# Kernel optimization log

Hardware: AMD Instinct MI355X
Metric: run time of the kernel (lower is better)

Reference implementation:

```python
import math
import jax, jax.numpy as jnp
import numpy as np

B, T, C, HS = 4, 4096, 2048, 128

def setup_inputs() -> dict:
    key = jax.random.key(0)
    k1, k2, k3, k4 = jax.random.split(key, 4)
    x = jax.random.normal(k1, (B, T, C), dtype=jnp.float32)
    # torch Linear init ~ U(-1/sqrt(in), 1/sqrt(in)); normal*0.02 is fine for a numeric baseline
    Wq = jax.random.normal(k2, (C, HS), dtype=jnp.float32) * 0.02
    Wk = jax.random.normal(k3, (C, HS), dtype=jnp.float32) * 0.02
    Wv = jax.random.normal(k4, (C, HS), dtype=jnp.float32) * 0.02
    return {"x": x, "Wq": Wq, "Wk": Wk, "Wv": Wv}

def reference(x, Wq, Wk, Wv):
    # Single-head causal self-attention (dropout in eval mode = identity).
    q = x @ Wq          # [B,T,HS]
    k = x @ Wk          # [B,T,HS]
    v = x @ Wv          # [B,T,HS]
    scale = 1.0 / math.sqrt(HS)
    att = jnp.einsum('bqd,bkd->bqk', q, k) * scale          # [B,T,T]
    causal = jnp.tril(jnp.ones((T, T), dtype=bool))          # [T,T]
    att = jnp.where(causal[None, :, :], att, -jnp.inf)
    att = jax.nn.softmax(att, axis=-1)
    y = jnp.einsum('bqk,bkd->bqd', att, v)                   # [B,T,HS]
    return y
```

## Files before the change

kernel.cpp:

```cpp
#include <hip/hip_runtime.h>
#include <hip/hip_bf16.h>


#define B_  4
#define T_  4096
#define C_  2048
#define HS_ 128

typedef unsigned short u16;
typedef __attribute__((ext_vector_type(8))) short short8;
typedef __attribute__((ext_vector_type(4))) float floatx4;

static __device__ __forceinline__ u16 f2bf(float x) {
  union { float f; unsigned u; } c; c.f = x;
  unsigned r = 0x7fffu + ((c.u >> 16) & 1u);
  return (u16)((c.u + r) >> 16);
}
static __device__ __forceinline__ u16 cvt_elem(float x) { return f2bf(x); }
static __device__ __forceinline__ u16 cvt_elem(u16 x) { return x; }

template <typename ST>
__global__ __launch_bounds__(256) void transpose_kernel(
    const ST* __restrict__ src, u16* __restrict__ dst, int R, int C) {
  __shared__ u16 tile[32][33];
  size_t moff = (size_t)blockIdx.z * (size_t)R * (size_t)C;
  src += moff; dst += moff;
  int c0 = blockIdx.x * 32, r0 = blockIdx.y * 32;
  int tx = threadIdx.x, ty = threadIdx.y;
#pragma unroll
  for (int i = 0; i < 4; ++i)
    tile[ty + 8 * i][tx] = cvt_elem(src[(size_t)(r0 + ty + 8 * i) * C + (c0 + tx)]);
  __syncthreads();
#pragma unroll
  for (int i = 0; i < 4; ++i)
    dst[(size_t)(c0 + ty + 8 * i) * R + (r0 + tx)] = tile[tx][ty + 8 * i];
}

#define GBM 128
#define GBK 64
#define LPAD 72

__global__ __launch_bounds__(256) void qkv_gemm_kernel(
    const float* __restrict__ X, const u16* __restrict__ WT3,
    u16* __restrict__ qkv) {
  __shared__ u16 Xs[GBM][LPAD];
  __shared__ u16 Ws[HS_][LPAD];
  int z = blockIdx.y;
  const u16* Wt = WT3 + (size_t)z * HS_ * C_;
  u16* outp = qkv + (size_t)z * ((size_t)B_ * T_ * HS_);
  int t = threadIdx.x;
  int wv = t >> 6, lane = t & 63;
  int l15 = lane & 15, hi = lane >> 4;
  int wm = (wv & 1) * 64, wn = (wv >> 1) * 64;
  size_t mbase = (size_t)blockIdx.x * GBM;

  floatx4 acc[4][4];
#pragma unroll
  for (int i = 0; i < 4; ++i)
#pragma unroll
    for (int j = 0; j < 4; ++j) acc[i][j] = (floatx4){0.f, 0.f, 0.f, 0.f};

  for (int kt = 0; kt < C_ / GBK; ++kt) {
#pragma unroll
    for (int i = 0; i < 4; ++i) {
      int id = i * 256 + t;
      int m = id >> 3, c = id & 7;
      const float* sp = &X[(mbase + m) * C_ + kt * GBK + c * 8];
      short8 v;
#pragma unroll
      for (int j = 0; j < 8; ++j) v[j] = (short)f2bf(sp[j]);
      *(short8*)&Xs[m][c * 8] = v;
    }
#pragma unroll
    for (int i = 0; i < 4; ++i) {
      int id = i * 256 + t;
      int n = id >> 3, c = id & 7;
      *(short8*)&Ws[n][c * 8] =
          *(const short8*)&Wt[(size_t)n * C_ + kt * GBK + c * 8];
    }
    __syncthreads();
#pragma unroll
    for (int ks = 0; ks < 2; ++ks) {
      short8 af[4], bf[4];
#pragma unroll
      for (int mt = 0; mt < 4; ++mt)
        af[mt] = *(const short8*)&Xs[wm + mt * 16 + l15][ks * 32 + hi * 8];
#pragma unroll
      for (int nt = 0; nt < 4; ++nt)
        bf[nt] = *(const short8*)&Ws[wn + nt * 16 + l15][ks * 32 + hi * 8];
#pragma unroll
      for (int mt = 0; mt < 4; ++mt)
#pragma unroll
        for (int nt = 0; nt < 4; ++nt)
          acc[mt][nt] = __builtin_amdgcn_mfma_f32_16x16x32_bf16(
              af[mt], bf[nt], acc[mt][nt], 0, 0, 0);
    }
    __syncthreads();
  }
#pragma unroll
  for (int mt = 0; mt < 4; ++mt)
#pragma unroll
    for (int nt = 0; nt < 4; ++nt)
#pragma unroll
      for (int r = 0; r < 4; ++r) {
        size_t row = mbase + wm + mt * 16 + hi * 4 + r;
        int col = wn + nt * 16 + l15;
        outp[row * HS_ + col] = f2bf(acc[mt][nt][r]);
      }
}

#define BQ 64
#define BKV 64
#define CHUNK 16

template <bool WRITE_PARTIAL>
static __device__ __forceinline__ void flash_body(
    const u16* __restrict__ q, const u16* __restrict__ k,
    const u16* __restrict__ vT, float* __restrict__ outO,
    float* __restrict__ Mp, float* __restrict__ Lp,
    int b, int qb, int kb0, int kb1, int slot) {
  __shared__ u16 Ks[BKV][136];
  __shared__ u16 Vs[HS_][72];
  __shared__ u16 Ps[BQ][72];
  int t = threadIdx.x;
  int wv = t >> 6, lane = t & 63, l15 = lane & 15, hi = lane >> 4;

  const float sc = 0.08838834764831845f * 1.4426950408889634f;

  short8 qf[4];
  {
    const u16* qrow = q + (size_t)(b * T_ + qb * BQ + wv * 16 + l15) * HS_;
#pragma unroll
    for (int ks = 0; ks < 4; ++ks)
      qf[ks] = *(const short8*)(qrow + ks * 32 + hi * 8);
  }

  floatx4 of[8];
#pragma unroll
  for (int dt = 0; dt < 8; ++dt) of[dt] = (floatx4){0.f, 0.f, 0.f, 0.f};
  float m_run[4], l_run[4];
#pragma unroll
  for (int r = 0; r < 4; ++r) { m_run[r] = -__builtin_inff(); l_run[r] = 0.f; }

  const u16* kbase = k + (size_t)b * T_ * HS_;
  const u16* vbase = vT + (size_t)b * HS_ * T_;

  for (int kb = kb0; kb <= kb1; ++kb) {
#pragma unroll
    for (int i = 0; i < 4; ++i) {
      int id = i * 256 + t;
      int n = id >> 4, c = id & 15;
      *(short8*)&Ks[n][c * 8] =
          *(const short8*)&kbase[(size_t)(kb * BKV + n) * HS_ + c * 8];
    }
#pragma unroll
    for (int i = 0; i < 4; ++i) {
      int id = i * 256 + t;
      int d = id >> 3, c = id & 7;
      *(short8*)&Vs[d][c * 8] =
          *(const short8*)&vbase[(size_t)d * T_ + kb * BKV + c * 8];
    }
    __syncthreads();

    floatx4 sf[4];
#pragma unroll
    for (int nt = 0; nt < 4; ++nt) {
      floatx4 s = (floatx4){0.f, 0.f, 0.f, 0.f};
#pragma unroll
      for (int ks = 0; ks < 4; ++ks) {
        short8 bfrag = *(const short8*)&Ks[nt * 16 + l15][ks * 32 + hi * 8];
        s = __builtin_amdgcn_mfma_f32_16x16x32_bf16(qf[ks], bfrag, s, 0, 0, 0);
      }
      sf[nt] = s;
    }

    float sv[4][4];
    if (kb == qb) {
#pragma unroll
      for (int nt = 0; nt < 4; ++nt) {
        int col = nt * 16 + l15;
#pragma unroll
        for (int r = 0; r < 4; ++r) {
          int row = wv * 16 + hi * 4 + r;
          sv[nt][r] = (col <= row) ? sf[nt][r] * sc : -__builtin_inff();
        }
      }
    } else {
#pragma unroll
      for (int nt = 0; nt < 4; ++nt)
#pragma unroll
        for (int r = 0; r < 4; ++r) sv[nt][r] = sf[nt][r] * sc;
    }

    float mt4[4], alpha[4];
#pragma unroll
    for (int r = 0; r < 4; ++r)
      mt4[r] = fmaxf(fmaxf(sv[0][r], sv[1][r]), fmaxf(sv[2][r], sv[3][r]));
#pragma unroll
    for (int off = 1; off < 16; off <<= 1)
#pragma unroll
      for (int r = 0; r < 4; ++r)
        mt4[r] = fmaxf(mt4[r], __shfl_xor(mt4[r], off));
#pragma unroll
    for (int r = 0; r < 4; ++r) {
      float mn = fmaxf(m_run[r], mt4[r]);
      alpha[r] = exp2f(m_run[r] - mn);
      m_run[r] = mn;
    }
    float pv[4][4], lt[4];
#pragma unroll
    for (int nt = 0; nt < 4; ++nt)
#pragma unroll
      for (int r = 0; r < 4; ++r) pv[nt][r] = exp2f(sv[nt][r] - m_run[r]);
#pragma unroll
    for (int r = 0; r < 4; ++r)
      lt[r] = (pv[0][r] + pv[1][r]) + (pv[2][r] + pv[3][r]);
#pragma unroll
    for (int off = 1; off < 16; off <<= 1)
#pragma unroll
      for (int r = 0; r < 4; ++r) lt[r] += __shfl_xor(lt[r], off);
#pragma unroll
    for (int r = 0; r < 4; ++r) l_run[r] = l_run[r] * alpha[r] + lt[r];
#pragma unroll
    for (int dt = 0; dt < 8; ++dt)
#pragma unroll
      for (int r = 0; r < 4; ++r) of[dt][r] *= alpha[r];

#pragma unroll
    for (int nt = 0; nt < 4; ++nt)
#pragma unroll
      for (int r = 0; r < 4; ++r)
        Ps[wv * 16 + hi * 4 + r][nt * 16 + l15] = f2bf(pv[nt][r]);
    __asm__ volatile("s_waitcnt lgkmcnt(0)" ::: "memory");

#pragma unroll
    for (int ks2 = 0; ks2 < 2; ++ks2) {
      short8 af = *(const short8*)&Ps[wv * 16 + l15][ks2 * 32 + hi * 8];
#pragma unroll
      for (int dt = 0; dt < 8; ++dt) {
        short8 bfrag = *(const short8*)&Vs[dt * 16 + l15][ks2 * 32 + hi * 8];
        of[dt] = __builtin_amdgcn_mfma_f32_16x16x32_bf16(af, bfrag, of[dt], 0, 0, 0);
      }
    }
    __syncthreads();
  }

  if (WRITE_PARTIAL) {
    float* Op = outO + (size_t)slot * (BQ * HS_);
#pragma unroll
    for (int dt = 0; dt < 8; ++dt)
#pragma unroll
      for (int r = 0; r < 4; ++r) {
        int row = wv * 16 + hi * 4 + r;
        Op[row * HS_ + dt * 16 + l15] = of[dt][r];
      }
    if (l15 == 0) {
#pragma unroll
      for (int r = 0; r < 4; ++r) {
        int row = wv * 16 + hi * 4 + r;
        Mp[slot * BQ + row] = m_run[r];
        Lp[slot * BQ + row] = l_run[r];
      }
    }
  } else {
    float rl[4];
#pragma unroll
    for (int r = 0; r < 4; ++r) rl[r] = 1.0f / l_run[r];
#pragma unroll
    for (int dt = 0; dt < 8; ++dt)
#pragma unroll
      for (int r = 0; r < 4; ++r) {
        size_t row = (size_t)(b * T_ + qb * BQ + wv * 16 + hi * 4 + r);
        outO[row * HS_ + dt * 16 + l15] = of[dt][r] * rl[r];
      }
  }
}

__global__ __launch_bounds__(256) void flash_partial_kernel(
    const u16* __restrict__ q, const u16* __restrict__ k,
    const u16* __restrict__ vT, float* __restrict__ Opart,
    float* __restrict__ Mpart, float* __restrict__ Lpart) {
  int qb = blockIdx.x, c = blockIdx.y, b = blockIdx.z;
  int kb0 = c * CHUNK;
  if (kb0 > qb) return;
  int kb1 = min(qb, kb0 + CHUNK - 1);
  int slot = (b * (T_ / BQ) + qb) * 4 + c;
  flash_body<true>(q, k, vT, Opart, Mpart, Lpart, b, qb, kb0, kb1, slot);
}

__global__ __launch_bounds__(256) void flash_attn_kernel(
    const u16* __restrict__ q, const u16* __restrict__ k,
    const u16* __restrict__ vT, float* __restrict__ out) {
  int qb = blockIdx.x, b = blockIdx.y;
  flash_body<false>(q, k, vT, out, nullptr, nullptr, b, qb, 0, qb, 0);
}

__global__ __launch_bounds__(256) void flash_merge_kernel(
    const float* __restrict__ Opart, const float* __restrict__ Mpart,
    const float* __restrict__ Lpart, float* __restrict__ out) {
  __shared__ float w[4][BQ];
  __shared__ float invL[BQ];
  int qb = blockIdx.x, b = blockIdx.y;
  int t = threadIdx.x;
  int nch = qb / CHUNK + 1;
  int slot0 = (b * (T_ / BQ) + qb) * 4;

  if (t < BQ) {
    float mv[4], mmax = -__builtin_inff();
    for (int c = 0; c < nch; ++c) {
      mv[c] = Mpart[(slot0 + c) * BQ + t];
      mmax = fmaxf(mmax, mv[c]);
    }
    float L = 0.f;
    for (int c = 0; c < nch; ++c) {
      float wc = exp2f(mv[c] - mmax);
      w[c][t] = wc;
      L += wc * Lpart[(slot0 + c) * BQ + t];
    }
    invL[t] = 1.0f / L;
  }
  __syncthreads();

  size_t obase = ((size_t)(b * T_) + (size_t)qb * BQ) * HS_;
#pragma unroll
  for (int j = 0; j < 32; ++j) {
    int e = j * 256 + t;
    int row = e >> 7;
    float acc = 0.f;
    for (int c = 0; c < nch; ++c)
      acc += w[c][row] * Opart[(size_t)(slot0 + c) * (BQ * HS_) + e];
    out[obase + e] = acc * invL[row];
  }
}

extern "C" void kernel_launch(void* const* d_in, const int* in_sizes, int n_in,
                              void* d_out, int out_size, void* d_ws, size_t ws_size,
                              hipStream_t stream) {
  const float* x  = (const float*)d_in[0];
  const float* Wq = (const float*)d_in[1];
  const float* Wk = (const float*)d_in[2];
  const float* Wv = (const float*)d_in[3];
  float* out = (float*)d_out;

  u16* ws = (u16*)d_ws;
  const size_t wtsz  = (size_t)HS_ * C_;
  const size_t qkvsz = (size_t)B_ * T_ * HS_;
  u16* WT = ws;
  u16* qv = WT + 3 * wtsz;
  u16* kv = qv + qkvsz;
  u16* vv = kv + qkvsz;
  u16* vT = vv + qkvsz;
  const size_t base_bytes = (3 * wtsz + 4 * qkvsz) * sizeof(u16);

  const int NSLOT = B_ * (T_ / BQ) * 4;
  float* Opart = (float*)((char*)d_ws + base_bytes);
  float* Mpart = Opart + (size_t)NSLOT * BQ * HS_;
  float* Lpart = Mpart + (size_t)NSLOT * BQ;
  const size_t split_bytes =
      base_bytes + ((size_t)NSLOT * BQ * HS_ + 2 * (size_t)NSLOT * BQ) * sizeof(float);

  dim3 tb(32, 8);
  transpose_kernel<float><<<dim3(HS_ / 32, C_ / 32, 1), tb, 0, stream>>>(Wq, WT + 0 * wtsz, C_, HS_);
  transpose_kernel<float><<<dim3(HS_ / 32, C_ / 32, 1), tb, 0, stream>>>(Wk, WT + 1 * wtsz, C_, HS_);
  transpose_kernel<float><<<dim3(HS_ / 32, C_ / 32, 1), tb, 0, stream>>>(Wv, WT + 2 * wtsz, C_, HS_);

  qkv_gemm_kernel<<<dim3((B_ * T_) / GBM, 3), 256, 0, stream>>>(x, WT, qv);

  transpose_kernel<u16><<<dim3(HS_ / 32, T_ / 32, B_), tb, 0, stream>>>(vv, vT, T_, HS_);

  if (ws_size >= split_bytes) {
    flash_partial_kernel<<<dim3(T_ / BQ, 4, B_), 256, 0, stream>>>(
        qv, kv, vT, Opart, Mpart, Lpart);
    flash_merge_kernel<<<dim3(T_ / BQ, B_), 256, 0, stream>>>(
        Opart, Mpart, Lpart, out);
  } else {
    flash_attn_kernel<<<dim3(T_ / BQ, B_), 256, 0, stream>>>(qv, kv, vT, out);
  }
}
```

Baseline: 352.3 us.

## Fuse QKV projections into one GEMM reading X once, writing V transposed

Replaces the three per-matrix QKV GEMM launches (each re-reading and converting X) with a single kernel that loads an X tile once and computes all 384 output columns, streaming weights directly from global memory instead of LDS. V is written already transposed, removing the separate V transpose kernel, and the three weight transposes are merged into one launch. The new GEMM uses small 32-row tiles with register prefetch of X, which cuts X traffic and launches but raises per-block weight reads from global/L2 and produces strided scattered stores for vT.

```diff
diff --git a/kernel.cpp b/kernel.cpp
--- a/kernel.cpp
+++ b/kernel.cpp
@@ -8,6 +8,7 @@
 #define HS_ 128
 
 typedef unsigned short u16;
+typedef __attribute__((ext_vector_type(4))) short short4v;
 typedef __attribute__((ext_vector_type(8))) short short8;
 typedef __attribute__((ext_vector_type(4))) float floatx4;
 
@@ -16,97 +17,94 @@
   unsigned r = 0x7fffu + ((c.u >> 16) & 1u);
   return (u16)((c.u + r) >> 16);
 }
-static __device__ __forceinline__ u16 cvt_elem(float x) { return f2bf(x); }
-static __device__ __forceinline__ u16 cvt_elem(u16 x) { return x; }
-
-template <typename ST>
-__global__ __launch_bounds__(256) void transpose_kernel(
-    const ST* __restrict__ src, u16* __restrict__ dst, int R, int C) {
+
+__global__ __launch_bounds__(256) void wtr_kernel(
+    const float* __restrict__ W0, const float* __restrict__ W1,
+    const float* __restrict__ W2, u16* __restrict__ WT) {
   __shared__ u16 tile[32][33];
-  size_t moff = (size_t)blockIdx.z * (size_t)R * (size_t)C;
-  src += moff; dst += moff;
+  int z = blockIdx.z;
+  const float* src = (z == 0) ? W0 : (z == 1) ? W1 : W2;
+  u16* dst = WT + (size_t)z * HS_ * C_;
   int c0 = blockIdx.x * 32, r0 = blockIdx.y * 32;
   int tx = threadIdx.x, ty = threadIdx.y;
 #pragma unroll
   for (int i = 0; i < 4; ++i)
-    tile[ty + 8 * i][tx] = cvt_elem(src[(size_t)(r0 + ty + 8 * i) * C + (c0 + tx)]);
+    tile[ty + 8 * i][tx] = f2bf(src[(size_t)(r0 + ty + 8 * i) * HS_ + (c0 + tx)]);
   __syncthreads();
 #pragma unroll
   for (int i = 0; i < 4; ++i)
-    dst[(size_t)(c0 + ty + 8 * i) * R + (r0 + tx)] = tile[tx][ty + 8 * i];
-}
-
-#define GBM 128
-#define GBK 64
-#define LPAD 72
-
-__global__ __launch_bounds__(256) void qkv_gemm_kernel(
+    dst[(size_t)(c0 + ty + 8 * i) * C_ + (r0 + tx)] = tile[tx][ty + 8 * i];
+}
+
+#define GBM 32
+#define GBK 32
+#define XPAD 40
+
+__global__ __launch_bounds__(256) void qkv_fused_kernel(
     const float* __restrict__ X, const u16* __restrict__ WT3,
-    u16* __restrict__ qkv) {
-  __shared__ u16 Xs[GBM][LPAD];
-  __shared__ u16 Ws[HS_][LPAD];
-  int z = blockIdx.y;
-  const u16* Wt = WT3 + (size_t)z * HS_ * C_;
-  u16* outp = qkv + (size_t)z * ((size_t)B_ * T_ * HS_);
+    u16* __restrict__ qv, u16* __restrict__ kv, u16* __restrict__ vT) {
+  __shared__ u16 Xs[GBM][XPAD];
   int t = threadIdx.x;
-  int wv = t >> 6, lane = t & 63;
-  int l15 = lane & 15, hi = lane >> 4;
-  int wm = (wv & 1) * 64, wn = (wv >> 1) * 64;
+  int wv = t >> 6, lane = t & 63, l15 = lane & 15, hi = lane >> 4;
+  int wn = wv * 96;
   size_t mbase = (size_t)blockIdx.x * GBM;
 
-  floatx4 acc[4][4];
-#pragma unroll
-  for (int i = 0; i < 4; ++i)
-#pragma unroll
-    for (int j = 0; j < 4; ++j) acc[i][j] = (floatx4){0.f, 0.f, 0.f, 0.f};
+  int sm = t >> 3, sc = (t & 7) * 4;
+  const float* xp = &X[(mbase + sm) * C_ + sc];
+
+  floatx4 acc[2][6];
+#pragma unroll
+  for (int i = 0; i < 2; ++i)
+#pragma unroll
+    for (int j = 0; j < 6; ++j) acc[i][j] = (floatx4){0.f, 0.f, 0.f, 0.f};
+
+  float4 xv = *(const float4*)xp;
 
   for (int kt = 0; kt < C_ / GBK; ++kt) {
-#pragma unroll
-    for (int i = 0; i < 4; ++i) {
-      int id = i * 256 + t;
-      int m = id >> 3, c = id & 7;
-      const float* sp = &X[(mbase + m) * C_ + kt * GBK + c * 8];
-      short8 v;
-#pragma unroll
-      for (int j = 0; j < 8; ++j) v[j] = (short)f2bf(sp[j]);
-      *(short8*)&Xs[m][c * 8] = v;
-    }
-#pragma unroll
-    for (int i = 0; i < 4; ++i) {
-      int id = i * 256 + t;
-      int n = id >> 3, c = id & 7;
-      *(short8*)&Ws[n][c * 8] =
-          *(const short8*)&Wt[(size_t)n * C_ + kt * GBK + c * 8];
-    }
+    short4v xs;
+    xs[0] = (short)f2bf(xv.x); xs[1] = (short)f2bf(xv.y);
+    xs[2] = (short)f2bf(xv.z); xs[3] = (short)f2bf(xv.w);
+    *(short4v*)&Xs[sm][sc] = xs;
+    if (kt + 1 < C_ / GBK) xv = *(const float4*)(xp + (kt + 1) * GBK);
     __syncthreads();
-#pragma unroll
-    for (int ks = 0; ks < 2; ++ks) {
-      short8 af[4], bf[4];
-#pragma unroll
-      for (int mt = 0; mt < 4; ++mt)
-        af[mt] = *(const short8*)&Xs[wm + mt * 16 + l15][ks * 32 + hi * 8];
-#pragma unroll
-      for (int nt = 0; nt < 4; ++nt)
-        bf[nt] = *(const short8*)&Ws[wn + nt * 16 + l15][ks * 32 + hi * 8];
-#pragma unroll
-      for (int mt = 0; mt < 4; ++mt)
-#pragma unroll
-        for (int nt = 0; nt < 4; ++nt)
-          acc[mt][nt] = __builtin_amdgcn_mfma_f32_16x16x32_bf16(
-              af[mt], bf[nt], acc[mt][nt], 0, 0, 0);
-    }
+
+    short8 bf[6];
+#pragma unroll
+    for (int nt = 0; nt < 6; ++nt)
+      bf[nt] = *(const short8*)&WT3[(size_t)(wn + nt * 16 + l15) * C_ + kt * GBK + hi * 8];
+    short8 af[2];
+#pragma unroll
+    for (int mt = 0; mt < 2; ++mt)
+      af[mt] = *(const short8*)&Xs[mt * 16 + l15][hi * 8];
+#pragma unroll
+    for (int mt = 0; mt < 2; ++mt)
+#pragma unroll
+      for (int nt = 0; nt < 6; ++nt)
+        acc[mt][nt] = __builtin_amdgcn_mfma_f32_16x16x32_bf16(
+            af[mt], bf[nt], acc[mt][nt], 0, 0, 0);
     __syncthreads();
   }
-#pragma unroll
-  for (int mt = 0; mt < 4; ++mt)
-#pragma unroll
-    for (int nt = 0; nt < 4; ++nt)
+
+#pragma unroll
+  for (int nt = 0; nt < 6; ++nt) {
+    int gcol = wn + nt * 16 + l15;
+    int z = gcol >> 7, lcol = gcol & 127;
+#pragma unroll
+    for (int mt = 0; mt < 2; ++mt)
 #pragma unroll
       for (int r = 0; r < 4; ++r) {
-        size_t row = mbase + wm + mt * 16 + hi * 4 + r;
-        int col = wn + nt * 16 + l15;
-        outp[row * HS_ + col] = f2bf(acc[mt][nt][r]);
-      }
+        size_t gt = mbase + mt * 16 + hi * 4 + r;
+        u16 val = f2bf(acc[mt][nt][r]);
+        if (z == 0) {
+          qv[gt * HS_ + lcol] = val;
+        } else if (z == 1) {
+          kv[gt * HS_ + lcol] = val;
+        } else {
+          size_t b = gt >> 12, tl = gt & (T_ - 1);
+          vT[b * (size_t)(HS_ * T_) + (size_t)lcol * T_ + tl] = val;
+        }
+      }
+  }
 }
 
 #define BQ 64
@@ -348,9 +346,8 @@
   u16* WT = ws;
   u16* qv = WT + 3 * wtsz;
   u16* kv = qv + qkvsz;
-  u16* vv = kv + qkvsz;
-  u16* vT = vv + qkvsz;
-  const size_t base_bytes = (3 * wtsz + 4 * qkvsz) * sizeof(u16);
+  u16* vT = kv + qkvsz;
+  const size_t base_bytes = (3 * wtsz + 3 * qkvsz) * sizeof(u16);
 
   const int NSLOT = B_ * (T_ / BQ) * 4;
   float* Opart = (float*)((char*)d_ws + base_bytes);
@@ -359,14 +356,9 @@
   const size_t split_bytes =
       base_bytes + ((size_t)NSLOT * BQ * HS_ + 2 * (size_t)NSLOT * BQ) * sizeof(float);
 
-  dim3 tb(32, 8);
-  transpose_kernel<float><<<dim3(HS_ / 32, C_ / 32, 1), tb, 0, stream>>>(Wq, WT + 0 * wtsz, C_, HS_);
-  transpose_kernel<float><<<dim3(HS_ / 32, C_ / 32, 1), tb, 0, stream>>>(Wk, WT + 1 * wtsz, C_, HS_);
-  transpose_kernel<float><<<dim3(HS_ / 32, C_ / 32, 1), tb, 0, stream>>>(Wv, WT + 2 * wtsz, C_, HS_);
-
-  qkv_gemm_kernel<<<dim3((B_ * T_) / GBM, 3), 256, 0, stream>>>(x, WT, qv);
-
-  transpose_kernel<u16><<<dim3(HS_ / 32, T_ / 32, B_), tb, 0, stream>>>(vv, vT, T_, HS_);
+  wtr_kernel<<<dim3(HS_ / 32, C_ / 32, 3), dim3(32, 8), 0, stream>>>(Wq, Wk, Wv, WT);
+
+  qkv_fused_kernel<<<(B_ * T_) / GBM, 256, 0, stream>>>(x, WT, qv, kv, vT);
 
   if (ws_size >= split_bytes) {
     flash_partial_kernel<<<dim3(T_ / BQ, 4, B_), 256, 0, stream>>>(
```

After: 397.8 us. +12.9%, slower.
